# Kernel optimization log

Measured on AMD Instinct MI355X. Metric: run time of the kernel, lower is better.

## Reference

```python
import jax, jax.numpy as jnp
import numpy as np

C = 256
R = 16
CR = C // R  # 16

def setup_inputs() -> dict:
    key = jax.random.key(0)
    k1, k2, k3 = jax.random.split(key, 3)
    x = jax.random.normal(k1, (16, C, 128, 128), dtype=jnp.float32)
    # 1x1 conv weights expressed as channel matmuls
    w1 = jax.random.normal(k2, (CR, C), dtype=jnp.float32) * (1.0 / np.sqrt(C))
    b1 = jnp.zeros((CR,), dtype=jnp.float32)
    w2 = jax.random.normal(k3, (C, CR), dtype=jnp.float32) * (1.0 / np.sqrt(CR))
    b2 = jnp.zeros((C,), dtype=jnp.float32)
    return {"x": x, "w1": w1, "b1": b1, "w2": w2, "b2": b2}

def reference(x, w1, b1, w2, b2):
    # global average pool over H,W -> [B, C]
    y = jnp.mean(x, axis=(2, 3))
    # 1x1 conv MLP: [B,C] @ [C,CR]^T -> relu -> [B,CR] @ [CR,C]^T -> sigmoid
    y = jax.nn.relu(jnp.einsum('bc,rc->br', y, w1) + b1)
    y = jax.nn.sigmoid(jnp.einsum('br,cr->bc', y, w2) + b2)
    # channel gating broadcast back onto x
    return x * y[:, :, None, None]
```

## Files before the change

### kernel.cpp

```cpp
#include <hip/hip_runtime.h>
#include <hip/hip_bf16.h>
#include <math.h>

#define PLANE 16384
#define PLANE4 4096
#define NPLANES 4096
#define NB 16
#define NC 256
#define NR 16

__global__ __launch_bounds__(256) void pool_kernel(const float* __restrict__ x,
                                                   float* __restrict__ mean) {
    const size_t base = (size_t)blockIdx.x * PLANE;
    const float4* xp = (const float4*)(x + base);
    float s = 0.f;
    #pragma unroll 4
    for (int i = threadIdx.x; i < PLANE4; i += 256) {
        float4 v = xp[i];
        s += (v.x + v.y) + (v.z + v.w);
    }
    #pragma unroll
    for (int o = 32; o > 0; o >>= 1) s += __shfl_down(s, o, 64);
    __shared__ float ws[4];
    if ((threadIdx.x & 63) == 0) ws[threadIdx.x >> 6] = s;
    __syncthreads();
    if (threadIdx.x == 0) {
        float t = (ws[0] + ws[1]) + (ws[2] + ws[3]);
        mean[blockIdx.x] = t * (1.0f / (float)PLANE);
    }
}

__global__ __launch_bounds__(256) void mlp_kernel(const float* __restrict__ mean,
                                                  const float* __restrict__ w1,
                                                  const float* __restrict__ b1,
                                                  const float* __restrict__ w2,
                                                  const float* __restrict__ b2,
                                                  float* __restrict__ gate) {
    __shared__ float ysh[NB * NC];
    __shared__ float hsh[NB * NR];
    for (int i = threadIdx.x; i < NB * NC; i += 256) ysh[i] = mean[i];
    __syncthreads();
    {
        const int b = threadIdx.x >> 4;
        const int r = threadIdx.x & 15;
        float acc = b1[r];
        #pragma unroll 8
        for (int c = 0; c < NC; ++c) acc += ysh[b * NC + c] * w1[r * NC + c];
        hsh[b * NR + r] = fmaxf(acc, 0.f);
    }
    __syncthreads();
    {
        const int c = threadIdx.x;
        const float bias = b2[c];
        float w2l[NR];
        #pragma unroll
        for (int r = 0; r < NR; ++r) w2l[r] = w2[c * NR + r];
        for (int b = 0; b < NB; ++b) {
            float a = bias;
            #pragma unroll
            for (int r = 0; r < NR; ++r) a += hsh[b * NR + r] * w2l[r];
            gate[b * NC + c] = 1.0f / (1.0f + expf(-a));
        }
    }
}

__global__ __launch_bounds__(256) void scale_kernel(const float* __restrict__ x,
                                                    const float* __restrict__ gate,
                                                    float* __restrict__ out) {
    const size_t base = (size_t)blockIdx.x * PLANE;
    const float g = gate[blockIdx.x];
    const float4* xp = (const float4*)(x + base);
    float4* op = (float4*)(out + base);
    #pragma unroll 4
    for (int i = threadIdx.x; i < PLANE4; i += 256) {
        float4 v = xp[i];
        v.x *= g; v.y *= g; v.z *= g; v.w *= g;
        op[i] = v;
    }
}

extern "C" void kernel_launch(void* const* d_in, const int* in_sizes, int n_in,
                              void* d_out, int out_size, void* d_ws, size_t ws_size,
                              hipStream_t stream) {
    const float* x  = (const float*)d_in[0];
    const float* w1 = (const float*)d_in[1];
    const float* b1 = (const float*)d_in[2];
    const float* w2 = (const float*)d_in[3];
    const float* b2 = (const float*)d_in[4];
    float* out = (float*)d_out;

    float* mean = (float*)d_ws;
    float* gate = mean + NPLANES;

    pool_kernel<<<NPLANES, 256, 0, stream>>>(x, mean);
    mlp_kernel<<<1, 256, 0, stream>>>(mean, w1, b1, w2, b2, gate);
    scale_kernel<<<NPLANES, 256, 0, stream>>>(x, gate, out);
}
```

Measured before the change: 505.2 us.

## Fuse SE MLP into scale kernel, reverse plane order, nontemporal stores

```diff
diff --git a/kernel.cpp b/kernel.cpp
--- a/kernel.cpp
+++ b/kernel.cpp
@@ -9,73 +9,77 @@
 #define NC 256
 #define NR 16
 
+typedef float vfloat4 __attribute__((ext_vector_type(4)));
+
 __global__ __launch_bounds__(256) void pool_kernel(const float* __restrict__ x,
                                                    float* __restrict__ mean) {
     const size_t base = (size_t)blockIdx.x * PLANE;
-    const float4* xp = (const float4*)(x + base);
+    const vfloat4* xp = (const vfloat4*)(x + base);
+    const int tid = threadIdx.x;
     float s = 0.f;
-    #pragma unroll 4
-    for (int i = threadIdx.x; i < PLANE4; i += 256) {
-        float4 v = xp[i];
+    #pragma unroll
+    for (int j = 0; j < 16; ++j) {
+        vfloat4 v = xp[tid + j * 256];
         s += (v.x + v.y) + (v.z + v.w);
     }
     #pragma unroll
     for (int o = 32; o > 0; o >>= 1) s += __shfl_down(s, o, 64);
-    __shared__ float ws[4];
-    if ((threadIdx.x & 63) == 0) ws[threadIdx.x >> 6] = s;
+    __shared__ float wsum[4];
+    if ((tid & 63) == 0) wsum[tid >> 6] = s;
     __syncthreads();
-    if (threadIdx.x == 0) {
-        float t = (ws[0] + ws[1]) + (ws[2] + ws[3]);
+    if (tid == 0) {
+        float t = (wsum[0] + wsum[1]) + (wsum[2] + wsum[3]);
         mean[blockIdx.x] = t * (1.0f / (float)PLANE);
     }
 }
 
-__global__ __launch_bounds__(256) void mlp_kernel(const float* __restrict__ mean,
-                                                  const float* __restrict__ w1,
-                                                  const float* __restrict__ b1,
-                                                  const float* __restrict__ w2,
-                                                  const float* __restrict__ b2,
-                                                  float* __restrict__ gate) {
-    __shared__ float ysh[NB * NC];
-    __shared__ float hsh[NB * NR];
-    for (int i = threadIdx.x; i < NB * NC; i += 256) ysh[i] = mean[i];
-    __syncthreads();
+__global__ __launch_bounds__(256) void scale_kernel(const float* __restrict__ x,
+                                                    const float* __restrict__ mean,
+                                                    const float* __restrict__ w1,
+                                                    const float* __restrict__ b1,
+                                                    const float* __restrict__ w2,
+                                                    const float* __restrict__ b2,
+                                                    float* __restrict__ out) {
+    const int plane = NPLANES - 1 - blockIdx.x;
+    const int b = plane >> 8;
+    const int c = plane & (NC - 1);
+    const int tid = threadIdx.x;
+    const int wave = tid >> 6;
+    const int lane = tid & 63;
+
+    __shared__ float hsh[NR];
+    __shared__ float gsh;
+
     {
-        const int b = threadIdx.x >> 4;
-        const int r = threadIdx.x & 15;
-        float acc = b1[r];
-        #pragma unroll 8
-        for (int c = 0; c < NC; ++c) acc += ysh[b * NC + c] * w1[r * NC + c];
-        hsh[b * NR + r] = fmaxf(acc, 0.f);
+        const vfloat4 yv = ((const vfloat4*)(mean + b * NC))[lane];
+        #pragma unroll
+        for (int k = 0; k < 4; ++k) {
+            const int r = wave * 4 + k;
+            const vfloat4 wv = ((const vfloat4*)(w1 + r * NC))[lane];
+            float p = yv.x * wv.x + yv.y * wv.y + yv.z * wv.z + yv.w * wv.w;
+            #pragma unroll
+            for (int o = 32; o > 0; o >>= 1) p += __shfl_down(p, o, 64);
+            if (lane == 0) hsh[r] = fmaxf(p + b1[r], 0.f);
+        }
     }
     __syncthreads();
-    {
-        const int c = threadIdx.x;
-        const float bias = b2[c];
-        float w2l[NR];
+    if (tid == 0) {
+        float a = b2[c];
         #pragma unroll
-        for (int r = 0; r < NR; ++r) w2l[r] = w2[c * NR + r];
-        for (int b = 0; b < NB; ++b) {
-            float a = bias;
-            #pragma unroll
-            for (int r = 0; r < NR; ++r) a += hsh[b * NR + r] * w2l[r];
-            gate[b * NC + c] = 1.0f / (1.0f + expf(-a));
-        }
+        for (int r = 0; r < NR; ++r) a += hsh[r] * w2[c * NR + r];
+        gsh = 1.0f / (1.0f + expf(-a));
     }
-}
+    __syncthreads();
+    const float g = gsh;
 
-__global__ __launch_bounds__(256) void scale_kernel(const float* __restrict__ x,
-                                                    const float* __restrict__ gate,
-                                                    float* __restrict__ out) {
-    const size_t base = (size_t)blockIdx.x * PLANE;
-    const float g = gate[blockIdx.x];
-    const float4* xp = (const float4*)(x + base);
-    float4* op = (float4*)(out + base);
-    #pragma unroll 4
-    for (int i = threadIdx.x; i < PLANE4; i += 256) {
-        float4 v = xp[i];
+    const size_t base = (size_t)plane * PLANE;
+    const vfloat4* xp = (const vfloat4*)(x + base);
+    vfloat4* op = (vfloat4*)(out + base);
+    #pragma unroll
+    for (int j = 0; j < 16; ++j) {
+        vfloat4 v = xp[tid + j * 256];
         v.x *= g; v.y *= g; v.z *= g; v.w *= g;
-        op[i] = v;
+        __builtin_nontemporal_store(v, op + tid + j * 256);
     }
 }
 
@@ -90,9 +94,7 @@
     float* out = (float*)d_out;
 
     float* mean = (float*)d_ws;
-    float* gate = mean + NPLANES;
 
     pool_kernel<<<NPLANES, 256, 0, stream>>>(x, mean);
-    mlp_kernel<<<1, 256, 0, stream>>>(mean, w1, b1, w2, b2, gate);
-    scale_kernel<<<NPLANES, 256, 0, stream>>>(x, gate, out);
+    scale_kernel<<<NPLANES, 256, 0, stream>>>(x, mean, w1, b1, w2, b2, out);
 }
```

Measured after the change: 481.6 us. -4.7%, faster.
